# Kernel optimization log

Measured on AMD Instinct MI355X. Metric: run time of the kernel, lower is better.

## Reference

```python
import math
import jax, jax.numpy as jnp
import numpy as np

B = 1024
C = 85742
M = 0.5
S = 64.0
COS_M = math.cos(M)
SIN_M = math.sin(M)
THRESHOLD = math.cos(math.pi - M)
MM = math.sin(math.pi - M) * M
T_MOMENTUM = 0.01  # t buffer starts at 0, so t = 0.01 * mean(target_logit)


def reference(logits, labels):
    # logits: [B, C] cosine similarities; labels: [B] int class ids
    rows = jnp.arange(logits.shape[0])
    target_logit = logits[rows, labels][:, None]                      # [B, 1]
    sin_theta = jnp.sqrt(1.0 - jnp.square(target_logit))
    cos_theta_m = target_logit * COS_M - sin_theta * SIN_M            # [B, 1]

    # hard-example mask computed against ORIGINAL logits (row-broadcast)
    mask = logits > cos_theta_m                                       # [B, C]

    final_target_logit = jnp.where(target_logit > THRESHOLD,
                                   cos_theta_m,
                                   target_logit - MM)                 # [B, 1]

    # running-stat t (torch.no_grad + buffer initialized to zero)
    t = jax.lax.stop_gradient(T_MOMENTUM * jnp.mean(target_logit))

    # reweight hard examples: logits[mask] = hard * (t + hard)
    new_logits = jnp.where(mask, logits * (t + logits), logits)       # [B, C]
    # scatter the margin-adjusted target logit back into the target column
    new_logits = new_logits.at[rows, labels].set(final_target_logit[:, 0])

    # numerator = s * target column; denominator = exp(numerator) + sum_{j != y} exp(s * logits_j)
    # since the target column now equals final_target_logit, this is exactly
    # the full-row sum-exp -> stable logsumexp over the whole row.
    numerator = S * final_target_logit[:, 0]                          # [B]
    log_denominator = jax.nn.logsumexp(S * new_logits, axis=1)        # [B]
    L = numerator - log_denominator
    return -jnp.mean(L)


def setup_inputs() -> dict:
    key = jax.random.key(0)
    k1, k2 = jax.random.split(key)
    # cosine-valued logits in (-0.99, 0.99) so sqrt(1 - t^2) is well-defined
    logits = jax.random.uniform(k1, (B, C), dtype=jnp.float32,
                                minval=-0.99, maxval=0.99)
    labels = jax.random.randint(k2, (B,), 0, C, dtype=jnp.int64)
    return {"logits": logits, "labels": labels}
```

## Files before the change

kernel.cpp:

```cpp
#include <hip/hip_runtime.h>
#include <math.h>


#define BB 1024
#define CC 85742
#define SS 64.0f
#define KCOS_M 0.8775825618903728f
#define KSIN_M 0.4794255386042030f
#define KTHRESH (-0.8775825618903728f)
#define KMM 0.2397127693021015f

__global__ __launch_bounds__(256) void cf_gather_kernel(
    const float* __restrict__ logits,
    const int* __restrict__ labels,
    float* __restrict__ sum_t) {
  const int row = blockIdx.x * 256 + threadIdx.x;
  float ty = logits[(size_t)row * CC + labels[row]];
  #pragma unroll
  for (int off = 32; off > 0; off >>= 1)
    ty += __shfl_down(ty, off, 64);
  __shared__ float wsum[4];
  const int lane = threadIdx.x & 63;
  const int wv = threadIdx.x >> 6;
  if (lane == 0) wsum[wv] = ty;
  __syncthreads();
  if (threadIdx.x == 0)
    atomicAdd(sum_t, wsum[0] + wsum[1] + wsum[2] + wsum[3]);
}

__global__ __launch_bounds__(256) void cf_row_kernel(
    const float* __restrict__ logits,
    const int* __restrict__ labels,
    const float* __restrict__ sum_t,
    float* __restrict__ out) {
  const int row = blockIdx.x;

  __shared__ float sh_ty, sh_t;
  if (threadIdx.x == 0) {
    sh_ty = logits[(size_t)row * CC + labels[row]];
    sh_t = 0.01f * (*sum_t) * (1.0f / BB);
  }
  __syncthreads();
  const float ty = sh_ty;
  const float t = sh_t;
  const float ctm = ty * KCOS_M - sqrtf(fmaxf(1.0f - ty * ty, 0.0f)) * KSIN_M;

  const float2* __restrict__ rowp =
      reinterpret_cast<const float2*>(logits + (size_t)row * CC);
  const int NV = CC / 2;

  float acc = 0.0f;
  for (int i = threadIdx.x; i < NV; i += 256) {
    const float2 v = rowp[i];
    const float x0 = v.x, x1 = v.y;
    const float n0 = (x0 > ctm) ? x0 * (t + x0) : x0;
    const float n1 = (x1 > ctm) ? x1 * (t + x1) : x1;
    acc += __expf(fmaf(SS, n0, -64.0f));
    acc += __expf(fmaf(SS, n1, -64.0f));
  }

  #pragma unroll
  for (int off = 32; off > 0; off >>= 1)
    acc += __shfl_down(acc, off, 64);
  __shared__ float wsum[4];
  const int lane = threadIdx.x & 63;
  const int wv = threadIdx.x >> 6;
  if (lane == 0) wsum[wv] = acc;
  __syncthreads();

  if (threadIdx.x == 0) {
    float sum = wsum[0] + wsum[1] + wsum[2] + wsum[3];
    const float modY = (ty > ctm) ? ty * (t + ty) : ty;
    const float finalT = (ty > KTHRESH) ? ctm : (ty - KMM);
    sum += __expf(fmaf(SS, finalT, -64.0f)) - __expf(fmaf(SS, modY, -64.0f));
    const float lse = logf(sum) + 64.0f;
    const float L = SS * finalT - lse;
    atomicAdd(out, -L * (1.0f / BB));
  }
}

extern "C" void kernel_launch(void* const* d_in, const int* in_sizes, int n_in,
                              void* d_out, int out_size, void* d_ws, size_t ws_size,
                              hipStream_t stream) {
  const float* logits = (const float*)d_in[0];
  const int* labels = (const int*)d_in[1];
  float* out = (float*)d_out;
  float* sum_t = (float*)d_ws;

  hipMemsetAsync(sum_t, 0, sizeof(float), stream);
  hipMemsetAsync(out, 0, sizeof(float), stream);

  cf_gather_kernel<<<BB / 256, 256, 0, stream>>>(logits, labels, sum_t);
  cf_row_kernel<<<BB, 256, 0, stream>>>(logits, labels, sum_t, out);
}
```

Before: 492.4 us.

## Fuse target gather into row kernel and vectorize row scan with float4 loads

Result: faster. 469.9 us (-4.6%).

```diff
diff --git a/kernel.cpp b/kernel.cpp
--- a/kernel.cpp
+++ b/kernel.cpp
@@ -9,70 +9,83 @@
 #define KSIN_M 0.4794255386042030f
 #define KTHRESH (-0.8775825618903728f)
 #define KMM 0.2397127693021015f
+#define K2E 92.33248261689366f
+#define NV4 21435
+#define STEP4 2048
+#define MAIN4 20480
 
-__global__ __launch_bounds__(256) void cf_gather_kernel(
+__device__ __forceinline__ float cf_elem(float x, float t, float ctm) {
+  const float n = (x > ctm) ? x * (t + x) : x;
+  return exp2f(fmaf(K2E, n, -K2E));
+}
+
+__global__ __launch_bounds__(256) void cf_fused_kernel(
     const float* __restrict__ logits,
     const int* __restrict__ labels,
-    float* __restrict__ sum_t) {
-  const int row = blockIdx.x * 256 + threadIdx.x;
-  float ty = logits[(size_t)row * CC + labels[row]];
+    float* __restrict__ out) {
+  const int row = blockIdx.x;
+  const int tid = threadIdx.x;
+  const int lane = tid & 63;
+  const int wv = tid >> 6;
+
+  __shared__ float wred[4];
+  __shared__ float sh_t, sh_ty;
+
+  float ts = 0.0f;
+  #pragma unroll
+  for (int k = 0; k < 4; ++k) {
+    const int r = tid * 4 + k;
+    ts += logits[(size_t)r * CC + labels[r]];
+  }
   #pragma unroll
   for (int off = 32; off > 0; off >>= 1)
-    ty += __shfl_down(ty, off, 64);
-  __shared__ float wsum[4];
-  const int lane = threadIdx.x & 63;
-  const int wv = threadIdx.x >> 6;
-  if (lane == 0) wsum[wv] = ty;
+    ts += __shfl_down(ts, off, 64);
+  if (lane == 0) wred[wv] = ts;
+  if (tid == 0) sh_ty = logits[(size_t)row * CC + labels[row]];
   __syncthreads();
-  if (threadIdx.x == 0)
-    atomicAdd(sum_t, wsum[0] + wsum[1] + wsum[2] + wsum[3]);
-}
+  if (tid == 0)
+    sh_t = 0.01f * (1.0f / BB) * ((wred[0] + wred[1]) + (wred[2] + wred[3]));
+  __syncthreads();
 
-__global__ __launch_bounds__(256) void cf_row_kernel(
-    const float* __restrict__ logits,
-    const int* __restrict__ labels,
-    const float* __restrict__ sum_t,
-    float* __restrict__ out) {
-  const int row = blockIdx.x;
-
-  __shared__ float sh_ty, sh_t;
-  if (threadIdx.x == 0) {
-    sh_ty = logits[(size_t)row * CC + labels[row]];
-    sh_t = 0.01f * (*sum_t) * (1.0f / BB);
-  }
-  __syncthreads();
+  const float t = sh_t;
   const float ty = sh_ty;
-  const float t = sh_t;
   const float ctm = ty * KCOS_M - sqrtf(fmaxf(1.0f - ty * ty, 0.0f)) * KSIN_M;
 
-  const float2* __restrict__ rowp =
-      reinterpret_cast<const float2*>(logits + (size_t)row * CC);
-  const int NV = CC / 2;
+  const float* __restrict__ base = logits + (size_t)row * CC;
+  const int mis = (row & 1) ? 2 : 0;
+  const float4* __restrict__ p4 = reinterpret_cast<const float4*>(base + mis);
 
   float acc = 0.0f;
-  for (int i = threadIdx.x; i < NV; i += 256) {
-    const float2 v = rowp[i];
-    const float x0 = v.x, x1 = v.y;
-    const float n0 = (x0 > ctm) ? x0 * (t + x0) : x0;
-    const float n1 = (x1 > ctm) ? x1 * (t + x1) : x1;
-    acc += __expf(fmaf(SS, n0, -64.0f));
-    acc += __expf(fmaf(SS, n1, -64.0f));
+  for (int b = 0; b < MAIN4; b += STEP4) {
+    float4 v[8];
+    #pragma unroll
+    for (int u = 0; u < 8; ++u) v[u] = p4[b + tid + u * 256];
+    #pragma unroll
+    for (int u = 0; u < 8; ++u)
+      acc += (cf_elem(v[u].x, t, ctm) + cf_elem(v[u].y, t, ctm)) +
+             (cf_elem(v[u].z, t, ctm) + cf_elem(v[u].w, t, ctm));
+  }
+  for (int i = MAIN4 + tid; i < NV4; i += 256) {
+    const float4 v = p4[i];
+    acc += (cf_elem(v.x, t, ctm) + cf_elem(v.y, t, ctm)) +
+           (cf_elem(v.z, t, ctm) + cf_elem(v.w, t, ctm));
+  }
+  if (tid == 0) {
+    const int i0 = mis ? 0 : (CC - 2);
+    acc += cf_elem(base[i0], t, ctm) + cf_elem(base[i0 + 1], t, ctm);
   }
 
   #pragma unroll
   for (int off = 32; off > 0; off >>= 1)
     acc += __shfl_down(acc, off, 64);
-  __shared__ float wsum[4];
-  const int lane = threadIdx.x & 63;
-  const int wv = threadIdx.x >> 6;
-  if (lane == 0) wsum[wv] = acc;
+  __syncthreads();
+  if (lane == 0) wred[wv] = acc;
   __syncthreads();
 
-  if (threadIdx.x == 0) {
-    float sum = wsum[0] + wsum[1] + wsum[2] + wsum[3];
-    const float modY = (ty > ctm) ? ty * (t + ty) : ty;
+  if (tid == 0) {
+    float sum = wred[0] + wred[1] + wred[2] + wred[3];
     const float finalT = (ty > KTHRESH) ? ctm : (ty - KMM);
-    sum += __expf(fmaf(SS, finalT, -64.0f)) - __expf(fmaf(SS, modY, -64.0f));
+    sum += exp2f(fmaf(K2E, finalT, -K2E)) - cf_elem(ty, t, ctm);
     const float lse = logf(sum) + 64.0f;
     const float L = SS * finalT - lse;
     atomicAdd(out, -L * (1.0f / BB));
@@ -85,11 +98,7 @@
   const float* logits = (const float*)d_in[0];
   const int* labels = (const int*)d_in[1];
   float* out = (float*)d_out;
-  float* sum_t = (float*)d_ws;
 
-  hipMemsetAsync(sum_t, 0, sizeof(float), stream);
   hipMemsetAsync(out, 0, sizeof(float), stream);
-
-  cf_gather_kernel<<<BB / 256, 256, 0, stream>>>(logits, labels, sum_t);
-  cf_row_kernel<<<BB, 256, 0, stream>>>(logits, labels, sum_t, out);
+  cf_fused_kernel<<<BB, 256, 0, stream>>>(logits, labels, out);
 }
```
